# Performance work log

Measured on AMD Instinct MI355X. Metric: run time of the kernel, lower is better.

## Reference

```python
import jax, jax.numpy as jnp
import numpy as np

NUM_CLASSES = 3
W_CE, W_DICE, W_LOVASZ, W_BOUNDARY, W_TOPO = 0.4, 0.3, 0.2, 0.08, 0.02
DICE_SMOOTH = 1e-5
LOVASZ_SUBSAMPLE_THRESH = 100000
LOVASZ_SUBSAMPLE_N = 50000


def _lovasz_hinge_flat(logits, fg):
    # logits, fg: [N]; fg in {0,1}. Sort errors descending, Lovasz gradient, dot.
    signs = 2.0 * fg - 1.0
    errors = 1.0 - logits * signs
    order = jnp.argsort(-errors)          # descending (stable)
    errors_sorted = errors[order]
    gt_sorted = fg[order]
    gts = gt_sorted.sum()
    intersection = gts - jnp.cumsum(gt_sorted)
    union = gts + jnp.cumsum(1.0 - gt_sorted)
    jaccard = 1.0 - intersection / jnp.maximum(union, 1e-12)
    jaccard = jnp.concatenate([jaccard[:1], jaccard[1:] - jaccard[:-1]])
    grad = jnp.where(gts > 0, jaccard, jnp.zeros_like(jaccard))  # gts==0 -> zero grad
    return jnp.dot(jax.nn.relu(errors_sorted), grad)


def structural_loss(predictions, labels):
    B, C, H, W = predictions.shape
    log_probs = jax.nn.log_softmax(predictions, axis=1)      # [B,C,H,W]
    probs = jnp.exp(log_probs)
    # ---- Cross entropy (mean) and per-pixel CE (reused by boundary loss) ----
    ce_pix = -jnp.take_along_axis(log_probs, labels[:, None, :, :], axis=1)[:, 0]  # [B,H,W]
    ce = ce_pix.mean()
    # ---- Dice loss (flattened over whole batch, per class) ----
    one_hot = jax.nn.one_hot(labels, C, dtype=probs.dtype, axis=1)  # [B,C,H,W]
    inter = jnp.sum(probs * one_hot, axis=(0, 2, 3))                 # [C]
    denom = jnp.sum(probs, axis=(0, 2, 3)) + jnp.sum(one_hot, axis=(0, 2, 3))
    dice_scores = (2.0 * inter + DICE_SMOOTH) / (denom + DICE_SMOOTH)
    dice = 1.0 - dice_scores.mean()
    # ---- Lovasz-Softmax ('present' classes, flat over batch, subsampled) ----
    p_flat = probs.transpose(0, 2, 3, 1).reshape(-1, C)  # [N,C]
    l_flat = labels.reshape(-1)                          # [N]
    N = l_flat.shape[0]
    lov_key = jax.random.key(42)
    losses, weights = [], []
    for c in range(C):
        fg_full = (l_flat == c).astype(probs.dtype)
        present = (fg_full.sum() > 0).astype(probs.dtype)
        logits_full = fg_full - p_flat[:, c]
        if N > LOVASZ_SUBSAMPLE_THRESH:
            idx = jax.random.permutation(jax.random.fold_in(lov_key, c), N)[:LOVASZ_SUBSAMPLE_N]
            logits_c, fg_c = logits_full[idx], fg_full[idx]
        else:
            logits_c, fg_c = logits_full, fg_full
        losses.append(_lovasz_hinge_flat(logits_c, fg_c))
        weights.append(present)
    losses = jnp.stack(losses)
    wts = jnp.stack(weights)
    lovasz = jnp.sum(losses * wts) / jnp.maximum(jnp.sum(wts), 1.0)
    # ---- Boundary loss: np.gradient-style boundary mask on classes {1,2} ----
    bnd = jnp.zeros(labels.shape, dtype=bool)
    for c in (1, 2):
        cm = (labels == c).astype(jnp.float32)          # [B,H,W]
        gx = jnp.abs(jnp.gradient(cm, axis=2))
        gy = jnp.abs(jnp.gradient(cm, axis=1))
        bnd = bnd | ((gx + gy) > 0.1)
    bmask = bnd.astype(predictions.dtype)
    boundary = jnp.sum(ce_pix * bmask) / (jnp.sum(bmask) + 1e-8)
    # ---- Topology loss (component count degenerates to presence indicator) ----
    topo = jnp.asarray(0.0, dtype=predictions.dtype)
    for c in (1, 2):
        gt_comp = jnp.any(labels == c, axis=(1, 2)).astype(predictions.dtype)      # [B]
        pred_comp = jnp.any(probs[:, c] > 0.5, axis=(1, 2)).astype(predictions.dtype)
        topo = topo + jnp.sum(jnp.maximum(pred_comp - gt_comp, 0.0) ** 2)
    topo = topo / B
    return (W_CE * ce + W_DICE * dice + W_LOVASZ * lovasz
            + W_BOUNDARY * boundary + W_TOPO * topo)


def setup_inputs() -> dict:
    key = jax.random.key(0)
    k1, k2 = jax.random.split(key)
    predictions = jax.random.normal(k1, (16, 3, 1024, 1024), dtype=jnp.float32)
    labels = jax.random.randint(k2, (16, 1024, 1024), 0, 3)
    return {"predictions": predictions, "labels": labels}


def reference(predictions, labels):
    return structural_loss(predictions, labels)
```

## Files before the change

### kernel.cpp

```cpp
#include <hip/hip_runtime.h>
#include <cstdint>
#include <cstddef>

#define K_BINS 1024
#define NBLK   1024
#define TPB    256
#define ROWS_PER_BLK 16
#define HW_    1048576u
#define W_     1024u
#define NPIX   16777216u
#define NHIST  (3*K_BINS)
#define NBLK_S (NBLK/8)

#define ZERO_BYTES 24704
#define PART_OFF   24832

#define GLD_LDS(SRC, DST)                                                      \
    __builtin_amdgcn_global_load_lds(                                          \
        (const __attribute__((address_space(1))) void*)(SRC),                  \
        (__attribute__((address_space(3))) void*)(DST), 16, 0, 0)

__device__ __forceinline__ void hist_add(unsigned int* h, int c, float e, int isfg) {
    int bin = (int)(e * (float)K_BINS);
    bin = bin < 0 ? 0 : (bin > K_BINS - 1 ? K_BINS - 1 : bin);
    atomicAdd(&h[c * K_BINS + bin], isfg ? 1u : 65536u);
}

__global__ __launch_bounds__(TPB, 4) void k_main(
    const float* __restrict__ pred, const int* __restrict__ lab,
    double* __restrict__ sums, unsigned long long* __restrict__ csums,
    unsigned int* __restrict__ finalhist, unsigned int* __restrict__ part, int use_dump)
{
    __shared__ float spbuf[2][3][1024];
    __shared__ unsigned int h[NHIST];
    __shared__ float redf[2][TPB / 64];
    __shared__ unsigned int redu[TPB / 64];
    __shared__ unsigned long long redl[TPB / 64];

    const int wv   = threadIdx.x >> 6;
    const int lane = threadIdx.x & 63;
    const bool do_hist = ((blockIdx.x & 7u) == 0u);

    const unsigned gr0   = blockIdx.x * ROWS_PER_BLK;
    const unsigned batch = gr0 >> 10;
    const unsigned i0    = gr0 & 1023u;
    const unsigned col   = threadIdx.x * 4u;
    const int*   labimg  = lab  + (size_t)batch * HW_;
    const float* predimg = pred + (size_t)(batch * 3u) * HW_;
    const unsigned bsh = batch * 4u;

#define STAGE(BB, TR)                                                          \
    {                                                                          \
        const unsigned gi = i0 + (unsigned)(TR);                               \
        _Pragma("unroll")                                                      \
        for (int s_ = 0; s_ < 3; ++s_) {                                       \
            const int k_ = wv * 3 + s_;                                        \
            const int c_ = k_ >> 2, q_ = k_ & 3;                               \
            const float* src_ = predimg + (size_t)c_ * HW_ + (size_t)gi * W_   \
                              + (unsigned)(q_ * 256 + lane * 4);               \
            GLD_LDS(src_, &spbuf[BB][c_][q_ * 256]);                           \
        }                                                                      \
    }

#define LROW(RR) (labimg + (size_t)((RR) < 0 ? 0 : ((RR) > 1023 ? 1023 : (RR))) * W_)

    STAGE(0, 0)
    const int ii0 = (int)i0;
    int4 lprev = *(const int4*)(LROW(ii0 - 1) + col);
    int4 lcur  = *(const int4*)(LROW(ii0)     + col);
    int4 lnext = *(const int4*)(LROW(ii0 + 1) + col);
    const bool has_lf = (col > 0u), has_rt = (col < 1020u);
    int lfA = has_lf ? LROW(ii0)[col - 1u] : 0;
    int rtA = has_rt ? LROW(ii0)[col + 4u] : 0;

    if (do_hist) {
        for (int idx = threadIdx.x; idx < NHIST; idx += TPB) h[idx] = 0u;
    }
    __syncthreads();

    float ce_acc = 0.f, bce_acc = 0.f;
    unsigned bcnt = 0;
    unsigned long long fl = 0ull;

#define PIXEL(A0, A1, A2, L, BND)                                              \
        {                                                                      \
            const float a0 = (A0), a1 = (A1), a2 = (A2); const int l = (L);    \
            const float m  = fmaxf(fmaxf(a0, a1), a2);                         \
            const float e0 = __expf(a0 - m), e1 = __expf(a1 - m), e2 = __expf(a2 - m); \
            const float s  = e0 + e1 + e2;                                     \
            const float lse = m + __logf(s);                                   \
            const float al = (l == 0) ? a0 : ((l == 1) ? a1 : a2);             \
            const float ce = lse - al;                                         \
            const float inv = __builtin_amdgcn_rcpf(s);                        \
            const float p0 = e0 * inv, p1 = e1 * inv, p2 = e2 * inv;           \
            ce_acc += ce;                                                      \
            if (BND) { bce_acc += ce; bcnt++; }                                \
            unsigned mbit = (l == 1 ? 1u : 0u) | (l == 2 ? 2u : 0u) |          \
                            (p1 > 0.5f ? 4u : 0u) | (p2 > 0.5f ? 8u : 0u);     \
            fl |= ((unsigned long long)mbit) << bsh;                           \
            if (do_hist) {                                                     \
                hist_add(h, 0, (l == 0) ? p0 : (1.0f - p0), l == 0);           \
                hist_add(h, 1, (l == 1) ? p1 : (1.0f - p1), l == 1);           \
                hist_add(h, 2, (l == 2) ? p2 : (1.0f - p2), l == 2);           \
            }                                                                  \
        }

    for (int r = 0; r < ROWS_PER_BLK; ++r) {
        int4 nlnext = lnext; int nlf = lfA, nrt = rtA;
        if (r < ROWS_PER_BLK - 1) {
            STAGE((r + 1) & 1, r + 1)
            nlnext = *(const int4*)(LROW(ii0 + r + 2) + col);
            nlf = has_lf ? LROW(ii0 + r + 1)[col - 1u] : 0;
            nrt = has_rt ? LROW(ii0 + r + 1)[col + 4u] : 0;
        }

        {
            const float* b0p = spbuf[r & 1][0];
            const float* b1p = spbuf[r & 1][1];
            const float* b2p = spbuf[r & 1][2];
            const float4 C0 = *(const float4*)(b0p + col);
            const float4 C1 = *(const float4*)(b1p + col);
            const float4 C2 = *(const float4*)(b2p + col);
            const int hd0 = (col == 0u)    ? (lcur.x != lcur.y) : (lfA != lcur.y);
            const int hd1 = (lcur.x != lcur.z);
            const int hd2 = (lcur.y != lcur.w);
            const int hd3 = (col == 1020u) ? (lcur.z != lcur.w) : (lcur.z != rtA);
            const int vd0 = (lprev.x != lnext.x), vd1 = (lprev.y != lnext.y);
            const int vd2 = (lprev.z != lnext.z), vd3 = (lprev.w != lnext.w);
            PIXEL(C0.x, C1.x, C2.x, lcur.x, (hd0 | vd0))
            PIXEL(C0.y, C1.y, C2.y, lcur.y, (hd1 | vd1))
            PIXEL(C0.z, C1.z, C2.z, lcur.z, (hd2 | vd2))
            PIXEL(C0.w, C1.w, C2.w, lcur.w, (hd3 | vd3))
        }

        __syncthreads();

        lprev = lcur; lcur = lnext; lnext = nlnext; lfA = nlf; rtA = nrt;
    }
#undef PIXEL
#undef STAGE
#undef LROW

#pragma unroll
    for (int off = 32; off; off >>= 1) {
        ce_acc  += __shfl_down(ce_acc, off);
        bce_acc += __shfl_down(bce_acc, off);
        bcnt    += __shfl_down(bcnt, off);
        fl      |= __shfl_down(fl, off);
    }
    if ((threadIdx.x & 63) == 0) {
        redf[0][wv] = ce_acc; redf[1][wv] = bce_acc;
        redu[wv] = bcnt;
        redl[wv] = fl;
    }
    __syncthreads();
    if (threadIdx.x == 0) {
        double a0 = 0, a1 = 0; unsigned int u = 0; unsigned long long L = 0ull;
        for (int w2 = 0; w2 < TPB / 64; w2++) {
            a0 += (double)redf[0][w2]; a1 += (double)redf[1][w2];
            u += redu[w2]; L |= redl[w2];
        }
        atomicAdd(&sums[0], a0);
        atomicAdd(&sums[1], a1);
        atomicAdd(&csums[0], (unsigned long long)u);
        atomicOr(&csums[1], L);
    }

    if (do_hist) {
        __syncthreads();
        if (use_dump) {
            unsigned int* dst = part + (size_t)(blockIdx.x >> 3) * NHIST;
            for (int idx = threadIdx.x; idx < NHIST; idx += TPB) dst[idx] = h[idx];
        } else {
            for (int idx = threadIdx.x; idx < NHIST; idx += TPB) {
                unsigned int v = h[idx];
                if (v & 0xFFFFu)  atomicAdd(&finalhist[idx * 2 + 0], v & 0xFFFFu);
                if (v >> 16)      atomicAdd(&finalhist[idx * 2 + 1], v >> 16);
            }
        }
    }
}

__global__ __launch_bounds__(256) void k_reduce(const unsigned int* __restrict__ part,
                                               unsigned int* __restrict__ finalhist)
{
    const int noch = NHIST / 256;
    const int och = blockIdx.x % noch;
    const int ich = blockIdx.x / noch;
    const int f = och * 256 + threadIdx.x;
    unsigned int lo = 0, hi = 0;
    const int b0 = ich * (NBLK_S / 8);
    for (int blk = b0; blk < b0 + NBLK_S / 8; ++blk) {
        const unsigned int v = part[(size_t)blk * NHIST + f];
        lo += v & 0xFFFFu;
        hi += v >> 16;
    }
    if (lo) atomicAdd(&finalhist[f * 2 + 0], lo);
    if (hi) atomicAdd(&finalhist[f * 2 + 1], hi);
}

__global__ __launch_bounds__(1024) void k_final(
    const double* __restrict__ sums, const unsigned long long* __restrict__ csums,
    const unsigned int* __restrict__ finalhist, float* __restrict__ out)
{
    __shared__ unsigned int sf[K_BINS], sb[K_BINS];
    __shared__ double red[16];
    __shared__ double red4[16][4];
    __shared__ double lres[3];
    __shared__ double dInter[3], dSumP[3], dCnt[3];
    const int t = threadIdx.x;

    for (int c = 0; c < 3; ++c) {
        const unsigned int fgc = finalhist[(c * K_BINS + t) * 2 + 0];
        const unsigned int bgc = finalhist[(c * K_BINS + t) * 2 + 1];
        sf[t] = fgc; sb[t] = bgc;

        const double ec = ((double)t + 0.5) / (double)K_BINS;
        double s0 = (double)fgc, s1 = (double)fgc * ec;
        double s2 = (double)bgc, s3 = (double)bgc * ec;
#pragma unroll
        for (int off = 32; off; off >>= 1) {
            s0 += __shfl_down(s0, off); s1 += __shfl_down(s1, off);
            s2 += __shfl_down(s2, off); s3 += __shfl_down(s3, off);
        }
        if ((t & 63) == 0) { red4[t >> 6][0] = s0; red4[t >> 6][1] = s1;
                             red4[t >> 6][2] = s2; red4[t >> 6][3] = s3; }
        __syncthreads();
        if (t == 0) {
            double cntf = 0, sfe = 0, cntb = 0, sbe = 0;
            for (int w2 = 0; w2 < 16; ++w2) {
                cntf += red4[w2][0]; sfe += red4[w2][1];
                cntb += red4[w2][2]; sbe += red4[w2][3];
            }
            const double inter = sfe;
            dInter[c] = inter;
            dSumP[c]  = inter + (cntb - sbe);
            dCnt[c]   = cntf;
        }
        __syncthreads();

        for (int off = 1; off < K_BINS; off <<= 1) {
            const unsigned int vf = sf[t] + ((t + off < K_BINS) ? sf[t + off] : 0u);
            const unsigned int vb = sb[t] + ((t + off < K_BINS) ? sb[t + off] : 0u);
            __syncthreads();
            sf[t] = vf; sb[t] = vb;
            __syncthreads();
        }
        const unsigned int gtsu = sf[0];
        double Jk = 0.0;
        if (t >= 1 && gtsu > 0u) {
            const double gts = (double)gtsu;
            Jk = 1.0 - (gts - (double)sf[t]) / (gts + (double)sb[t]);
        }
#pragma unroll
        for (int off = 32; off; off >>= 1) Jk += __shfl_down(Jk, off);
        if ((t & 63) == 0) red[t >> 6] = Jk;
        __syncthreads();
        if (t == 0) {
            double sj = 0; for (int w2 = 0; w2 < 16; ++w2) sj += red[w2];
            lres[c] = (gtsu > 0u) ? ((0.5 + sj) / (double)K_BINS) : -1.0;
        }
        __syncthreads();
    }

    if (t == 0) {
        const double N = 16777216.0;
        const double ce = sums[0] / N;
        double dsum = 0.0;
        for (int c = 0; c < 3; c++) {
            dsum += (2.0 * dInter[c] + 1e-5) / (dSumP[c] + dCnt[c] + 1e-5);
        }
        const double dice = 1.0 - dsum / 3.0;
        double lsum = 0.0, wsum = 0.0;
        for (int c = 0; c < 3; c++) {
            if (lres[c] >= 0.0) { lsum += lres[c]; wsum += 1.0; }
        }
        const double lovasz = lsum / fmax(wsum, 1.0);
        const double bnd = sums[1] / ((double)csums[0] + 1e-8);
        const unsigned long long fl = csums[1];
        double topo = 0.0;
        for (int b = 0; b < 16; b++) {
            for (int c2 = 0; c2 < 2; c2++) {
                const double gt = (double)((fl >> (b * 4 + c2)) & 1ull);
                const double pr = (double)((fl >> (b * 4 + 2 + c2)) & 1ull);
                const double d = pr - gt;
                if (d > 0.0) topo += d * d;
            }
        }
        topo /= 16.0;
        out[0] = (float)(0.4 * ce + 0.3 * dice + 0.2 * lovasz + 0.08 * bnd + 0.02 * topo);
    }
}

extern "C" void kernel_launch(void* const* d_in, const int* in_sizes, int n_in,
                              void* d_out, int out_size, void* d_ws, size_t ws_size,
                              hipStream_t stream)
{
    const float* pred = (const float*)d_in[0];
    const int*   lab  = (const int*)d_in[1];
    float* out = (float*)d_out;

    char* wsb = (char*)d_ws;
    double* sums = (double*)wsb;
    unsigned long long* csums = (unsigned long long*)(wsb + 64);
    unsigned int* finalhist = (unsigned int*)(wsb + 128);
    unsigned int* part = (unsigned int*)(wsb + PART_OFF);
    const size_t need = (size_t)PART_OFF + (size_t)NBLK_S * NHIST * 4u;
    const int use_dump = (ws_size >= need) ? 1 : 0;

    hipMemsetAsync(d_ws, 0, ZERO_BYTES, stream);
    hipLaunchKernelGGL(k_main, dim3(NBLK), dim3(TPB), 0, stream,
                       pred, lab, sums, csums, finalhist, part, use_dump);
    if (use_dump)
        hipLaunchKernelGGL(k_reduce, dim3(96), dim3(256), 0, stream, part, finalhist);
    hipLaunchKernelGGL(k_final, dim3(1), dim3(1024), 0, stream, sums, csums, finalhist, out);
}
```

Baseline: 88.98 us.

## Replace global atomics with per-block partials, halve histogram bins, double block count

Each block now writes its CE, boundary and flag partials to its own workspace slot, and k_final reduces them, replacing global double and 64-bit atomics. The main grid doubles to 2048 blocks of 8 rows, and the Lovasz histogram shrinks to 512 bins. In dump mode k_reduce writes the final histogram directly, so the memset is skipped. Fewer bins coarsen the Lovasz approximation, and the hidden part of k_main must still be consistent with the new row count.

```diff
diff --git a/kernel.cpp b/kernel.cpp
--- a/kernel.cpp
+++ b/kernel.cpp
@@ -2,18 +2,21 @@
 #include <cstdint>
 #include <cstddef>
 
-#define K_BINS 1024
-#define NBLK   1024
+#define K_BINS 512
+#define NBLK   2048
 #define TPB    256
-#define ROWS_PER_BLK 16
+#define ROWS_PER_BLK 8
 #define HW_    1048576u
 #define W_     1024u
 #define NPIX   16777216u
 #define NHIST  (3*K_BINS)
 #define NBLK_S (NBLK/8)
 
-#define ZERO_BYTES 24704
-#define PART_OFF   24832
+#define PA_OFF   0
+#define PU_OFF   32768
+#define PL_OFF   49152
+#define FH_OFF   65536
+#define PART_OFF 81920
 
 #define GLD_LDS(SRC, DST)                                                      \
     __builtin_amdgcn_global_load_lds(                                          \
@@ -28,7 +31,8 @@
 
 __global__ __launch_bounds__(TPB, 4) void k_main(
     const float* __restrict__ pred, const int* __restrict__ lab,
-    double* __restrict__ sums, unsigned long long* __restrict__ csums,
+    double* __restrict__ pa, unsigned long long* __restrict__ pu,
+    unsigned long long* __restrict__ pl,
     unsigned int* __restrict__ finalhist, unsigned int* __restrict__ part, int use_dump)
 {
     __shared__ float spbuf[2][3][1024];
@@ -160,10 +164,10 @@
             a0 += (double)redf[0][w2]; a1 += (double)redf[1][w2];
             u += redu[w2]; L |= redl[w2];
         }
-        atomicAdd(&sums[0], a0);
-        atomicAdd(&sums[1], a1);
-        atomicAdd(&csums[0], (unsigned long long)u);
-        atomicOr(&csums[1], L);
+        pa[blockIdx.x * 2 + 0] = a0;
+        pa[blockIdx.x * 2 + 1] = a1;
+        pu[blockIdx.x] = (unsigned long long)u;
+        pl[blockIdx.x] = L;
     }
 
     if (do_hist) {
@@ -184,23 +188,20 @@
 __global__ __launch_bounds__(256) void k_reduce(const unsigned int* __restrict__ part,
                                                unsigned int* __restrict__ finalhist)
 {
-    const int noch = NHIST / 256;
-    const int och = blockIdx.x % noch;
-    const int ich = blockIdx.x / noch;
-    const int f = och * 256 + threadIdx.x;
+    const int f = blockIdx.x * 256 + threadIdx.x;
     unsigned int lo = 0, hi = 0;
-    const int b0 = ich * (NBLK_S / 8);
-    for (int blk = b0; blk < b0 + NBLK_S / 8; ++blk) {
+    for (int blk = 0; blk < NBLK_S; ++blk) {
         const unsigned int v = part[(size_t)blk * NHIST + f];
         lo += v & 0xFFFFu;
         hi += v >> 16;
     }
-    if (lo) atomicAdd(&finalhist[f * 2 + 0], lo);
-    if (hi) atomicAdd(&finalhist[f * 2 + 1], hi);
+    finalhist[f * 2 + 0] = lo;
+    finalhist[f * 2 + 1] = hi;
 }
 
 __global__ __launch_bounds__(1024) void k_final(
-    const double* __restrict__ sums, const unsigned long long* __restrict__ csums,
+    const double* __restrict__ pa, const unsigned long long* __restrict__ pu,
+    const unsigned long long* __restrict__ pl,
     const unsigned int* __restrict__ finalhist, float* __restrict__ out)
 {
     __shared__ unsigned int sf[K_BINS], sb[K_BINS];
@@ -208,16 +209,49 @@
     __shared__ double red4[16][4];
     __shared__ double lres[3];
     __shared__ double dInter[3], dSumP[3], dCnt[3];
+    __shared__ double tot[3];
+    __shared__ unsigned long long totL;
     const int t = threadIdx.x;
 
+    {
+        double a0 = pa[t * 2 + 0] + pa[(t + 1024) * 2 + 0];
+        double a1 = pa[t * 2 + 1] + pa[(t + 1024) * 2 + 1];
+        double uu = (double)pu[t] + (double)pu[t + 1024];
+        unsigned long long L = pl[t] | pl[t + 1024];
+#pragma unroll
+        for (int off = 32; off; off >>= 1) {
+            a0 += __shfl_down(a0, off);
+            a1 += __shfl_down(a1, off);
+            uu += __shfl_down(uu, off);
+            L  |= __shfl_down(L, off);
+        }
+        if ((t & 63) == 0) { red4[t >> 6][0] = a0; red4[t >> 6][1] = a1;
+                             red4[t >> 6][2] = uu;
+                             red[t >> 6] = __longlong_as_double((long long)L); }
+        __syncthreads();
+        if (t == 0) {
+            double s0 = 0, s1 = 0, s2 = 0; unsigned long long LL = 0ull;
+            for (int w2 = 0; w2 < 16; ++w2) {
+                s0 += red4[w2][0]; s1 += red4[w2][1]; s2 += red4[w2][2];
+                LL |= (unsigned long long)__double_as_longlong(red[w2]);
+            }
+            tot[0] = s0; tot[1] = s1; tot[2] = s2; totL = LL;
+        }
+        __syncthreads();
+    }
+
     for (int c = 0; c < 3; ++c) {
-        const unsigned int fgc = finalhist[(c * K_BINS + t) * 2 + 0];
-        const unsigned int bgc = finalhist[(c * K_BINS + t) * 2 + 1];
-        sf[t] = fgc; sb[t] = bgc;
-
+        unsigned int fgc = 0, bgc = 0;
+        if (t < K_BINS) {
+            fgc = finalhist[(c * K_BINS + t) * 2 + 0];
+            bgc = finalhist[(c * K_BINS + t) * 2 + 1];
+            sf[t] = fgc; sb[t] = bgc;
+        }
         const double ec = ((double)t + 0.5) / (double)K_BINS;
-        double s0 = (double)fgc, s1 = (double)fgc * ec;
-        double s2 = (double)bgc, s3 = (double)bgc * ec;
+        double s0 = (t < K_BINS) ? (double)fgc : 0.0;
+        double s1 = (t < K_BINS) ? (double)fgc * ec : 0.0;
+        double s2 = (t < K_BINS) ? (double)bgc : 0.0;
+        double s3 = (t < K_BINS) ? (double)bgc * ec : 0.0;
 #pragma unroll
         for (int off = 32; off; off >>= 1) {
             s0 += __shfl_down(s0, off); s1 += __shfl_down(s1, off);
@@ -240,15 +274,18 @@
         __syncthreads();
 
         for (int off = 1; off < K_BINS; off <<= 1) {
-            const unsigned int vf = sf[t] + ((t + off < K_BINS) ? sf[t + off] : 0u);
-            const unsigned int vb = sb[t] + ((t + off < K_BINS) ? sb[t + off] : 0u);
+            unsigned int vf = 0, vb = 0;
+            if (t < K_BINS) {
+                vf = sf[t] + ((t + off < K_BINS) ? sf[t + off] : 0u);
+                vb = sb[t] + ((t + off < K_BINS) ? sb[t + off] : 0u);
+            }
             __syncthreads();
-            sf[t] = vf; sb[t] = vb;
+            if (t < K_BINS) { sf[t] = vf; sb[t] = vb; }
             __syncthreads();
         }
         const unsigned int gtsu = sf[0];
         double Jk = 0.0;
-        if (t >= 1 && gtsu > 0u) {
+        if (t >= 1 && t < K_BINS && gtsu > 0u) {
             const double gts = (double)gtsu;
             Jk = 1.0 - (gts - (double)sf[t]) / (gts + (double)sb[t]);
         }
@@ -265,7 +302,7 @@
 
     if (t == 0) {
         const double N = 16777216.0;
-        const double ce = sums[0] / N;
+        const double ce = tot[0] / N;
         double dsum = 0.0;
         for (int c = 0; c < 3; c++) {
             dsum += (2.0 * dInter[c] + 1e-5) / (dSumP[c] + dCnt[c] + 1e-5);
@@ -276,8 +313,8 @@
             if (lres[c] >= 0.0) { lsum += lres[c]; wsum += 1.0; }
         }
         const double lovasz = lsum / fmax(wsum, 1.0);
-        const double bnd = sums[1] / ((double)csums[0] + 1e-8);
-        const unsigned long long fl = csums[1];
+        const double bnd = tot[1] / (tot[2] + 1e-8);
+        const unsigned long long fl = totL;
         double topo = 0.0;
         for (int b = 0; b < 16; b++) {
             for (int c2 = 0; c2 < 2; c2++) {
@@ -301,17 +338,20 @@
     float* out = (float*)d_out;
 
     char* wsb = (char*)d_ws;
-    double* sums = (double*)wsb;
-    unsigned long long* csums = (unsigned long long*)(wsb + 64);
-    unsigned int* finalhist = (unsigned int*)(wsb + 128);
+    double* pa = (double*)(wsb + PA_OFF);
+    unsigned long long* pu = (unsigned long long*)(wsb + PU_OFF);
+    unsigned long long* pl = (unsigned long long*)(wsb + PL_OFF);
+    unsigned int* finalhist = (unsigned int*)(wsb + FH_OFF);
     unsigned int* part = (unsigned int*)(wsb + PART_OFF);
     const size_t need = (size_t)PART_OFF + (size_t)NBLK_S * NHIST * 4u;
     const int use_dump = (ws_size >= need) ? 1 : 0;
 
-    hipMemsetAsync(d_ws, 0, ZERO_BYTES, stream);
+    if (!use_dump)
+        hipMemsetAsync(finalhist, 0, NHIST * 2 * sizeof(unsigned int), stream);
+
     hipLaunchKernelGGL(k_main, dim3(NBLK), dim3(TPB), 0, stream,
-                       pred, lab, sums, csums, finalhist, part, use_dump);
+                       pred, lab, pa, pu, pl, finalhist, part, use_dump);
     if (use_dump)
-        hipLaunchKernelGGL(k_reduce, dim3(96), dim3(256), 0, stream, part, finalhist);
-    hipLaunchKernelGGL(k_final, dim3(1), dim3(1024), 0, stream, sums, csums, finalhist, out);
-}
+        hipLaunchKernelGGL(k_reduce, dim3(NHIST / 256), dim3(256), 0, stream, part, finalhist);
+    hipLaunchKernelGGL(k_final, dim3(1), dim3(1024), 0, stream, pa, pu, pl, finalhist, out);
+}
```

Result: faster. 87.14 us (-2.1%).
